# Kernel optimization log

Hardware: AMD Instinct MI355X
Metric: run time of the kernel (lower is better)

## Reference

```python
import jax, jax.numpy as jnp
import numpy as np

D = 256; H = 8; L = 4; K = 4; AS = 2; HD = D // H
KK = K * K
LEVEL_SHAPES = [(128, 128), (64, 64), (32, 32), (16, 16)]


def _kernel_indices():
    # kernel_size=4 (even): linspace(-1.5, 1.5, 4); stack [j, i] then / K
    idx = jnp.linspace(-1.5, 1.5, K)
    ii, jj = jnp.meshgrid(idx, idx, indexing='ij')
    return jnp.stack([jj, ii], axis=-1).reshape(-1, 2) / K  # (KK, 2)


def _bilinear(vf, g, Hl, Wl):
    # vf: (b, H, Hl*Wl, HD) per-level value; g: (b, l1, H, KK, 2) in [0,1]
    # grid_sample semantics, align_corners=False, zero padding
    b, l1, h, kk, _ = g.shape
    x = g[..., 0] * Wl - 0.5
    y = g[..., 1] * Hl - 0.5
    x0 = jnp.floor(x)
    y0 = jnp.floor(y)
    acc = None
    for dx, dy in ((0, 0), (1, 0), (0, 1), (1, 1)):
        xi = x0 + dx
        yi = y0 + dy
        w = (1.0 - jnp.abs(x - xi)) * (1.0 - jnp.abs(y - yi))
        valid = (xi >= 0) & (xi < Wl) & (yi >= 0) & (yi < Hl)
        idx = (jnp.clip(yi, 0, Hl - 1) * Wl + jnp.clip(xi, 0, Wl - 1)).astype(jnp.int32)
        idx = idx.transpose(0, 2, 1, 3).reshape(b, h, l1 * kk)
        gth = jnp.take_along_axis(vf, idx[..., None], axis=2)  # (b,H,l1*kk,HD)
        ww = (w * valid).transpose(0, 2, 1, 3).reshape(b, h, l1 * kk)
        c = gth * ww[..., None]
        acc = c if acc is None else acc + c
    return acc.reshape(b, h, l1, kk, HD).transpose(0, 2, 1, 3, 4)  # (b,l1,H,kk,HD)


def setup_inputs() -> dict:
    key = jax.random.key(0)
    ks = jax.random.split(key, 9)
    b, l1 = 4, 1024
    l2 = sum(h * w for h, w in LEVEL_SHAPES)  # 21760
    query = jax.random.normal(ks[0], (b, l1, D), jnp.float32)
    value = jax.random.normal(ks[1], (b, l2, D), jnp.float32)
    centers = jax.random.uniform(ks[2], (b, l1, 2), jnp.float32)
    sizes = jax.random.uniform(ks[3], (b, l1, 2), jnp.float32) * 0.2 + 0.05
    ref_windows = jnp.concatenate([centers, sizes], axis=-1)  # (b,l1,4) cx,cy,w,h
    s = 1.0 / np.sqrt(D)
    Wv = jax.random.normal(ks[4], (D, D), jnp.float32) * s
    bv = jnp.zeros((D,), jnp.float32)
    Wo = jax.random.normal(ks[5], (D, D), jnp.float32) * s
    bo = jnp.zeros((D,), jnp.float32)
    Wbox = jax.random.normal(ks[6], (L * H * 4, D), jnp.float32) * 0.01
    bbox = jax.random.uniform(ks[7], (H * L * 4,), jnp.float32)
    Wattn = jax.random.normal(ks[8], (H * L * AS * AS, D), jnp.float32) * s
    battn = jnp.zeros((H * L * AS * AS,), jnp.float32)
    v_shape = np.array(LEVEL_SHAPES, np.int64)
    starts = np.cumsum([0] + [h * w for h, w in LEVEL_SHAPES[:-1]])
    v_start_index = np.array(starts, np.int64)
    v_mask = jnp.zeros((b, l2), bool)
    return dict(query=query, value=value, ref_windows=ref_windows, Wv=Wv, bv=bv,
                Wo=Wo, bo=bo, Wbox=Wbox, bbox=bbox, Wattn=Wattn, battn=battn,
                v_shape=v_shape, v_start_index=v_start_index, v_mask=v_mask)


def reference(query, value, ref_windows, Wv, bv, Wo, bo, Wbox, bbox, Wattn, battn,
              v_shape, v_start_index, v_mask):
    b, l1, _ = query.shape
    l2 = value.shape[1]
    # value projection + padding mask
    v = value @ Wv.T + bv
    v = jnp.where(v_mask[..., None], 0.0, v).reshape(b, l2, H, HD)
    # where to attend: offset boxes -> sampling grid (normalizer=None branch)
    off = (query @ Wbox.T + bbox).reshape(b, l1, H, L, 4)
    refw = ref_windows[:, :, None, None, :]            # (b,l1,1,1,4)
    refsz = jnp.concatenate([refw[..., 2:4], refw[..., 2:4]], axis=-1)
    boxes = refw + off / 8.0 * refsz                   # (b,l1,H,L,4)
    center = boxes[..., None, :2]
    size = boxes[..., None, 2:]
    grid = center + _kernel_indices() * jax.nn.relu(size)  # (b,l1,H,L,KK,2)
    # attention weights (attn_size grid upsampled to kernel_size by repeat_interleave)
    aw = (query @ Wattn.T + battn).reshape(b, l1, H, L, AS, AS)
    nr = K // AS
    aw = jnp.repeat(jnp.repeat(aw, nr, axis=-1), nr, axis=-2)  # (b,l1,H,L,K,K)
    sw = jax.nn.softmax(aw.reshape(b, l1, H, -1), axis=-1).reshape(b, l1, H, L, KK)
    lw = jax.nn.softmax(aw, axis=3).reshape(b, l1, H, L, KK)
    out = jnp.zeros((b, l1, H, HD), query.dtype)
    mout = jnp.zeros((b, l1, H, HD), query.dtype)
    for li in range(L):
        Hl, Wl = int(v_shape[li, 0]), int(v_shape[li, 1])
        st = int(v_start_index[li])
        vf = v[:, st:st + Hl * Wl].transpose(0, 2, 1, 3)  # (b,H,Hl*Wl,HD)
        samp = _bilinear(vf, grid[:, :, :, li], Hl, Wl)   # (b,l1,H,KK,HD)
        out = out + jnp.einsum('bqhkd,bqhk->bqhd', samp, sw[:, :, :, li])
        mout = mout + jnp.einsum('bqhkd,bqhk->bqhd', samp, lw[:, :, :, li])
    out = out.reshape(b, l1, D) @ Wo.T + bo
    mout = mout.reshape(b, l1, D) @ Wo.T + bo
    return out, mout, aw
```

## Files before the change

kernel.cpp:

```cpp
#include <hip/hip_runtime.h>
#include <hip/hip_bf16.h>


typedef __attribute__((ext_vector_type(8))) short short8;
typedef __attribute__((ext_vector_type(4))) float f32x4;
typedef __attribute__((ext_vector_type(4))) unsigned int uint4v;

__device__ __forceinline__ unsigned short f2bf(float f) {
    unsigned int u = __float_as_uint(f);
    unsigned int r = u + 0x7FFFu + ((u >> 16) & 1u);
    return (unsigned short)(r >> 16);
}
__device__ __forceinline__ unsigned int pkbf(float a, float b) {
    __hip_bfloat162 h = __float22bfloat162_rn(float2{a, b});
    return *reinterpret_cast<unsigned int*>(&h);
}
__device__ __forceinline__ short8 pack2(float4 x, float4 y) {
    uint4v u;
    u[0] = pkbf(x.x, x.y); u[1] = pkbf(x.z, x.w);
    u[2] = pkbf(y.x, y.y); u[3] = pkbf(y.z, y.w);
    return __builtin_bit_cast(short8, u);
}
__device__ __forceinline__ void gld_lds16(const float* g, float* l) {
    __builtin_amdgcn_global_load_lds(
        (const __attribute__((address_space(1))) unsigned int*)g,
        (__attribute__((address_space(3))) unsigned int*)l, 16, 0, 0);
}

__device__ __forceinline__ void storeC(float* C, size_t i, float v) { C[i] = v; }
__device__ __forceinline__ void storeC(unsigned short* C, size_t i, float v) { C[i] = f2bf(v); }

template <typename OutT>
__device__ __forceinline__ void gemm_body2(
    const float* __restrict__ A, const float* __restrict__ W,
    const float* __restrict__ bias, OutT* __restrict__ C,
    int N, int bm, int bn, float* AsF, float* WsF)
{
    const int tid  = threadIdx.x;
    const int lane = tid & 63;
    const int wave = tid >> 6;
    const int wm = (wave & 1) * 64;
    const int wn = (wave >> 1) * 64;
    const int kg = lane >> 4;
    const int lm = lane & 15;

    f32x4 acc[4][4];
#pragma unroll
    for (int i = 0; i < 4; ++i)
#pragma unroll
        for (int j = 0; j < 4; ++j) {
            acc[i][j][0] = 0.f; acc[i][j][1] = 0.f;
            acc[i][j][2] = 0.f; acc[i][j][3] = 0.f;
        }

    const int g = (lane & 7) ^ (lane >> 3);
    const float* Ag = A + (size_t)(bm + 32 * wave + (lane >> 3)) * 256 + 4 * g;
    const float* Wg = W + (size_t)(bn + 32 * wave + (lane >> 3)) * 256 + 4 * g;
    float* Al = AsF + (32 * wave) * 32;
    float* Wl = WsF + (32 * wave) * 32;

    const int p0 = (2 * kg) ^ (lm & 7);
    const int p1 = p0 ^ 1;
    const float4* Af4 = (const float4*)AsF;
    const float4* Wf4 = (const float4*)WsF;
    const int abase = (wm + lm) * 8;
    const int bbase = (wn + lm) * 8;

    for (int k0 = 0; k0 < 256; k0 += 32) {
        __syncthreads();
#pragma unroll
        for (int j = 0; j < 4; ++j) {
            gld_lds16(Ag + (size_t)j * 8 * 256 + k0, Al + j * 8 * 32);
            gld_lds16(Wg + (size_t)j * 8 * 256 + k0, Wl + j * 8 * 32);
        }
        __syncthreads();
        short8 af[4], bfr[4];
#pragma unroll
        for (int i = 0; i < 4; ++i) {
            float4 c0 = Af4[abase + i * 128 + p0];
            float4 c1 = Af4[abase + i * 128 + p1];
            af[i] = pack2(c0, c1);
        }
#pragma unroll
        for (int j = 0; j < 4; ++j) {
            float4 c0 = Wf4[bbase + j * 128 + p0];
            float4 c1 = Wf4[bbase + j * 128 + p1];
            bfr[j] = pack2(c0, c1);
        }
#pragma unroll
        for (int i = 0; i < 4; ++i)
#pragma unroll
            for (int j = 0; j < 4; ++j)
                acc[i][j] = __builtin_amdgcn_mfma_f32_16x16x32_bf16(
                    af[i], bfr[j], acc[i][j], 0, 0, 0);
    }

#pragma unroll
    for (int j = 0; j < 4; ++j) {
        int col = bn + wn + j * 16 + lm;
        float bcol = bias[col];
#pragma unroll
        for (int i = 0; i < 4; ++i) {
#pragma unroll
            for (int r = 0; r < 4; ++r) {
                int row = bm + wm + i * 16 + kg * 4 + r;
                storeC(C, (size_t)row * N + col, acc[i][j][r] + bcol);
            }
        }
    }
}

#define LDA 56

__device__ __forceinline__ void gemm_body_f32(
    const float* __restrict__ A, const float* __restrict__ W,
    const float* __restrict__ bias, float* __restrict__ C,
    int N, int bm, int bn, unsigned short* As, unsigned short* Ws)
{
    const int tid  = threadIdx.x;
    const int lane = tid & 63;
    const int wave = tid >> 6;
    const int wm = (wave & 1) * 64;
    const int wn = (wave >> 1) * 64;
    const int lr = tid >> 1;
    const int lh = (tid & 1) * 16;
    const int kg = lane >> 4;
    const int lm = lane & 15;

    f32x4 acc[4][4];
#pragma unroll
    for (int i = 0; i < 4; ++i)
#pragma unroll
        for (int j = 0; j < 4; ++j) {
            acc[i][j][0] = 0.f; acc[i][j][1] = 0.f;
            acc[i][j][2] = 0.f; acc[i][j][3] = 0.f;
        }

    const float* Ap = A + (size_t)(bm + lr) * 256 + lh;
    const float* Wp = W + (size_t)(bn + lr) * 256 + lh;
    unsigned short* Asp = &As[lr * LDA + lh];
    unsigned short* Wsp = &Ws[lr * LDA + lh];

    for (int k0 = 0; k0 < 256; k0 += 32) {
        float4 a0 = *(const float4*)(Ap + k0);
        float4 a1 = *(const float4*)(Ap + k0 + 4);
        float4 a2 = *(const float4*)(Ap + k0 + 8);
        float4 a3 = *(const float4*)(Ap + k0 + 12);
        float4 w0 = *(const float4*)(Wp + k0);
        float4 w1 = *(const float4*)(Wp + k0 + 4);
        float4 w2 = *(const float4*)(Wp + k0 + 8);
        float4 w3 = *(const float4*)(Wp + k0 + 12);
        __syncthreads();
        *(short8*)(Asp)     = pack2(a0, a1);
        *(short8*)(Asp + 8) = pack2(a2, a3);
        *(short8*)(Wsp)     = pack2(w0, w1);
        *(short8*)(Wsp + 8) = pack2(w2, w3);
        __syncthreads();
        short8 af[4], bfr[4];
#pragma unroll
        for (int i = 0; i < 4; ++i)
            af[i] = *(const short8*)&As[(wm + i * 16 + lm) * LDA + kg * 8];
#pragma unroll
        for (int j = 0; j < 4; ++j)
            bfr[j] = *(const short8*)&Ws[(wn + j * 16 + lm) * LDA + kg * 8];
#pragma unroll
        for (int i = 0; i < 4; ++i)
#pragma unroll
            for (int j = 0; j < 4; ++j)
                acc[i][j] = __builtin_amdgcn_mfma_f32_16x16x32_bf16(
                    af[i], bfr[j], acc[i][j], 0, 0, 0);
    }

#pragma unroll
    for (int j = 0; j < 4; ++j) {
        int col = bn + wn + j * 16 + lm;
        float bcol = bias[col];
#pragma unroll
        for (int i = 0; i < 4; ++i)
#pragma unroll
            for (int r = 0; r < 4; ++r) {
                int row = bm + wm + i * 16 + kg * 4 + r;
                C[(size_t)row * N + col] = acc[i][j][r] + bcol;
            }
    }
}

__device__ __forceinline__ void gemm_body_bf16A(
    const unsigned short* __restrict__ A, const float* __restrict__ W,
    const float* __restrict__ bias, float* __restrict__ C,
    int N, int bm, int bn, unsigned short* As, unsigned short* Ws)
{
    const int tid  = threadIdx.x;
    const int lane = tid & 63;
    const int wave = tid >> 6;
    const int wm = (wave & 1) * 64;
    const int wn = (wave >> 1) * 64;
    const int lr = tid >> 1;
    const int lh = (tid & 1) * 16;
    const int kg = lane >> 4;
    const int lm = lane & 15;

    f32x4 acc[4][4];
#pragma unroll
    for (int i = 0; i < 4; ++i)
#pragma unroll
        for (int j = 0; j < 4; ++j) {
            acc[i][j][0] = 0.f; acc[i][j][1] = 0.f;
            acc[i][j][2] = 0.f; acc[i][j][3] = 0.f;
        }

    const unsigned short* Ap = A + (size_t)(bm + lr) * 256 + lh;
    const float* Wp = W + (size_t)(bn + lr) * 256 + lh;
    unsigned short* Asp = &As[lr * LDA + lh];
    unsigned short* Wsp = &Ws[lr * LDA + lh];

    for (int k0 = 0; k0 < 256; k0 += 32) {
        uint4v a01 = *(const uint4v*)(Ap + k0);
        uint4v a23 = *(const uint4v*)(Ap + k0 + 8);
        float4 w0 = *(const float4*)(Wp + k0);
        float4 w1 = *(const float4*)(Wp + k0 + 4);
        float4 w2 = *(const float4*)(Wp + k0 + 8);
        float4 w3 = *(const float4*)(Wp + k0 + 12);
        __syncthreads();
        *(short8*)(Asp)     = __builtin_bit_cast(short8, a01);
        *(short8*)(Asp + 8) = __builtin_bit_cast(short8, a23);
        *(short8*)(Wsp)     = pack2(w0, w1);
        *(short8*)(Wsp + 8) = pack2(w2, w3);
        __syncthreads();
        short8 af[4], bfr[4];
#pragma unroll
        for (int i = 0; i < 4; ++i)
            af[i] = *(const short8*)&As[(wm + i * 16 + lm) * LDA + kg * 8];
#pragma unroll
        for (int j = 0; j < 4; ++j)
            bfr[j] = *(const short8*)&Ws[(wn + j * 16 + lm) * LDA + kg * 8];
#pragma unroll
        for (int i = 0; i < 4; ++i)
#pragma unroll
            for (int j = 0; j < 4; ++j)
                acc[i][j] = __builtin_amdgcn_mfma_f32_16x16x32_bf16(
                    af[i], bfr[j], acc[i][j], 0, 0, 0);
    }

#pragma unroll
    for (int j = 0; j < 4; ++j) {
        int col = bn + wn + j * 16 + lm;
        float bcol = bias[col];
#pragma unroll
        for (int i = 0; i < 4; ++i)
#pragma unroll
            for (int r = 0; r < 4; ++r) {
                int row = bm + wm + i * 16 + kg * 4 + r;
                C[(size_t)row * N + col] = acc[i][j][r] + bcol;
            }
    }
}

__global__ __launch_bounds__(256) void gemm_vq_kernel(
    const float* __restrict__ value, const float* __restrict__ Wv,
    const float* __restrict__ bv, unsigned short* __restrict__ v,
    const float* __restrict__ query,
    const float* __restrict__ Wbox, const float* __restrict__ bbox, float* __restrict__ off,
    const float* __restrict__ Wattn, const float* __restrict__ battn, float* __restrict__ awr)
{
    __shared__ __align__(16) char smem[32768];
    const int x = blockIdx.x;
    if (x < 1360) {
        gemm_body2<unsigned short>(value, Wv, bv, v, 256,
                                   (x >> 1) * 128, (x & 1) * 128,
                                   (float*)smem, (float*)(smem + 16384));
    } else {
        const int idx = x - 1360;
        const int bm = (idx & 31) * 128;
        unsigned short* As = (unsigned short*)smem;
        unsigned short* Ws = As + 128 * LDA;
        if (idx < 32) gemm_body_f32(query, Wbox, bbox, off, 128, bm, 0, As, Ws);
        else          gemm_body_f32(query, Wattn, battn, awr, 128, bm, 0, As, Ws);
    }
}

__global__ __launch_bounds__(256) void gemm_o_kernel(
    const unsigned short* __restrict__ A, const float* __restrict__ W,
    const float* __restrict__ bias, float* __restrict__ C)
{
    __shared__ __align__(16) unsigned short As[128 * LDA];
    __shared__ __align__(16) unsigned short Ws[128 * LDA];
    gemm_body_bf16A(A, W, bias, C, 256, blockIdx.x * 128, blockIdx.y * 128, As, Ws);
}

__global__ __launch_bounds__(512, 8) void sample_kernel(
    const unsigned short* __restrict__ v, const float* __restrict__ off,
    const float* __restrict__ awr, const float* __restrict__ refw,
    float* __restrict__ aw_out, unsigned short* __restrict__ accb)
{
    const int x  = blockIdx.x;
    const int bq = ((x & 3) << 10) | (x >> 2);
    const int b  = bq >> 10;
    const int t  = threadIdx.x;

    __shared__ float ref4[4];
    __shared__ float awl[128];
    __shared__ float bxs[128];
    __shared__ float swl[512];
    __shared__ float lwl[512];
    __shared__ int4  tp[32 * 66];

    if (t < 4)   ref4[t] = refw[bq * 4 + t];
    if (t < 128) awl[t] = awr[(size_t)bq * 128 + t];
    __syncthreads();

    if (t < 128) {
        float o = off[(size_t)bq * 128 + t];
        int comp = t & 3;
        float r0 = ref4[0], r1 = ref4[1], r2 = ref4[2], r3 = ref4[3];
        float bx;
        if (comp == 0)      bx = r0 + o * 0.125f * r2;
        else if (comp == 1) bx = r1 + o * 0.125f * r3;
        else if (comp == 2) bx = r2 + o * 0.125f * r2;
        else                bx = r3 + o * 0.125f * r3;
        bxs[t] = bx;

        const int h = t >> 4, r = t & 15;
        float a = awl[t];
        float m = a;
#pragma unroll
        for (int s = 1; s < 16; s <<= 1) m = fmaxf(m, __shfl_xor(m, s, 16));
        float se = expf(a - m);
#pragma unroll
        for (int s = 1; s < 16; s <<= 1) se += __shfl_xor(se, s, 16);
        const float inv_s = 1.0f / (4.0f * se);

        float* awq = aw_out + (size_t)bq * 512 + h * 64;
#pragma unroll
        for (int j = 0; j < 4; ++j) {
            int eidx = r * 4 + j;
            int l  = eidx >> 4;
            int ky = (eidx >> 2) & 3;
            int kx = eidx & 3;
            int pos = (ky >> 1) * 2 + (kx >> 1);
            float raw = awl[h * 16 + l * 4 + pos];
            swl[h * 64 + eidx] = expf(raw - m) * inv_s;
            int base = h * 16 + pos;
            float m2 = awl[base];
#pragma unroll
            for (int li = 1; li < 4; ++li) m2 = fmaxf(m2, awl[base + li * 4]);
            float s2 = 0.f;
#pragma unroll
            for (int li = 0; li < 4; ++li) s2 += expf(awl[base + li * 4] - m2);
            lwl[h * 64 + eidx] = expf(raw - m2) / s2;
            awq[eidx] = raw;
        }
    }
    __syncthreads();

    {
        const int STs_[4] = {0, 16384, 20480, 21504};
        int e = t;
        int eh = e >> 6, rem = e & 63, l = rem >> 4, kk = rem & 15;
        const float* bx = &bxs[eh * 16 + l * 4];
        float cx = bx[0], cy = bx[1];
        float bw = fmaxf(bx[2], 0.f), bh = fmaxf(bx[3], 0.f);
        float kx = -0.375f + 0.25f * (float)(kk & 3);
        float ky = -0.375f + 0.25f * (float)(kk >> 2);
        int Wl = 128 >> l;
        float xg = (cx + kx * bw) * (float)Wl - 0.5f;
        float yg = (cy + ky * bh) * (float)Wl - 0.5f;
        float x0f = floorf(xg), y0f = floorf(yg);
        int x0 = (int)x0f, y0 = (int)y0f;
        float fx = xg - x0f, fy = yg - y0f;
        float sww = swl[e], lww = lwl[e];
        int rowbase = b * 21760 + STs_[l];
        int4* dst = &tp[(eh * 4 + l) * 66 + kk * 4];
#pragma unroll
        for (int tap = 0; tap < 4; ++tap) {
            int dx = tap & 1, dy = tap >> 1;
            int xi = x0 + dx, yi = y0 + dy;
            float w = (dx ? fx : 1.f - fx) * (dy ? fy : 1.f - fy);
            if (xi < 0 || xi >= Wl || yi < 0 || yi >= Wl) w = 0.f;
            int xc = min(max(xi, 0), Wl - 1);
            int yc = min(max(yi, 0), Wl - 1);
            dst[tap] = int4{(rowbase + yc * Wl + xc) << 6,
                            __float_as_int(w * sww),
                            __float_as_int(w * lww), 0};
        }
    }
    __syncthreads();

    const int h    = t >> 6;
    const int lane = t & 63;
    const int l    = (lane >> 4) & 3;
    const int sub  = (lane >> 3) & 1;
    const int cl   = lane & 7;
    const uint2* vp = (const uint2*)v;
    const int choff = h * 8 + cl;
    const int4* sp = &tp[(h * 4 + l) * 66 + sub];

    float a0 = 0.f, a1 = 0.f, a2 = 0.f, a3 = 0.f;
    float m0 = 0.f, m1 = 0.f, m2 = 0.f, m3 = 0.f;
#pragma unroll 4
    for (int i = 0; i < 32; ++i) {
        int4 d = sp[2 * i];
        uint2 pv = vp[(size_t)(d.x + choff)];
        float v0 = __uint_as_float(pv.x << 16);
        float v1 = __uint_as_float(pv.x & 0xffff0000u);
        float v2 = __uint_as_float(pv.y << 16);
        float v3 = __uint_as_float(pv.y & 0xffff0000u);
        float wo = __int_as_float(d.y), wm = __int_as_float(d.z);
        a0 = fmaf(v0, wo, a0); a1 = fmaf(v1, wo, a1);
        a2 = fmaf(v2, wo, a2); a3 = fmaf(v3, wo, a3);
        m0 = fmaf(v0, wm, m0); m1 = fmaf(v1, wm, m1);
        m2 = fmaf(v2, wm, m2); m3 = fmaf(v3, wm, m3);
    }
#pragma unroll
    for (int s = 8; s <= 32; s <<= 1) {
        a0 += __shfl_xor(a0, s); a1 += __shfl_xor(a1, s);
        a2 += __shfl_xor(a2, s); a3 += __shfl_xor(a3, s);
        m0 += __shfl_xor(m0, s); m1 += __shfl_xor(m1, s);
        m2 += __shfl_xor(m2, s); m3 += __shfl_xor(m3, s);
    }
    if (lane < 8) {
        size_t base = (size_t)bq * 256 + h * 32 + cl * 4;
        *(uint2*)&accb[base] = uint2{pkbf(a0, a1), pkbf(a2, a3)};
        *(uint2*)&accb[base + (size_t)4096 * 256] = uint2{pkbf(m0, m1), pkbf(m2, m3)};
    }
}

extern "C" void kernel_launch(void* const* d_in, const int* in_sizes, int n_in,
                              void* d_out, int out_size, void* d_ws, size_t ws_size,
                              hipStream_t stream) {
    const float* query = (const float*)d_in[0];
    const float* value = (const float*)d_in[1];
    const float* refw  = (const float*)d_in[2];
    const float* Wv    = (const float*)d_in[3];
    const float* bv    = (const float*)d_in[4];
    const float* Wo    = (const float*)d_in[5];
    const float* bo    = (const float*)d_in[6];
    const float* Wbox  = (const float*)d_in[7];
    const float* bbox  = (const float*)d_in[8];
    const float* Wattn = (const float*)d_in[9];
    const float* battn = (const float*)d_in[10];

    float* out = (float*)d_out;
    float* aw_out = out + 2 * 1048576;

    unsigned short* v = (unsigned short*)d_ws;
    float* off = (float*)((char*)d_ws + 44564480);
    float* awr = off + 524288;
    unsigned short* accb = (unsigned short*)(awr + 524288);

    gemm_vq_kernel<<<1424, 256, 0, stream>>>(value, Wv, bv, v,
                                             query, Wbox, bbox, off,
                                             Wattn, battn, awr);
    sample_kernel<<<4096, 512, 0, stream>>>(v, off, awr, refw, aw_out, accb);
    gemm_o_kernel<<<dim3(64, 2), 256, 0, stream>>>(accb, Wo, bo, out);
}
```

Baseline: 250.2 us.

## Double-buffer LDS tiles in value projection GEMM to overlap loads with MFMA

```diff
diff --git a/kernel.cpp b/kernel.cpp
--- a/kernel.cpp
+++ b/kernel.cpp
@@ -29,6 +29,8 @@
 
 __device__ __forceinline__ void storeC(float* C, size_t i, float v) { C[i] = v; }
 __device__ __forceinline__ void storeC(unsigned short* C, size_t i, float v) { C[i] = f2bf(v); }
+
+#define TILE_F 4096
 
 template <typename OutT>
 __device__ __forceinline__ void gemm_body2(
@@ -56,24 +58,37 @@
     const int g = (lane & 7) ^ (lane >> 3);
     const float* Ag = A + (size_t)(bm + 32 * wave + (lane >> 3)) * 256 + 4 * g;
     const float* Wg = W + (size_t)(bn + 32 * wave + (lane >> 3)) * 256 + 4 * g;
-    float* Al = AsF + (32 * wave) * 32;
-    float* Wl = WsF + (32 * wave) * 32;
+    const int ldsw = (32 * wave) * 32;
 
     const int p0 = (2 * kg) ^ (lm & 7);
     const int p1 = p0 ^ 1;
-    const float4* Af4 = (const float4*)AsF;
-    const float4* Wf4 = (const float4*)WsF;
     const int abase = (wm + lm) * 8;
     const int bbase = (wn + lm) * 8;
 
-    for (int k0 = 0; k0 < 256; k0 += 32) {
-        __syncthreads();
-#pragma unroll
-        for (int j = 0; j < 4; ++j) {
-            gld_lds16(Ag + (size_t)j * 8 * 256 + k0, Al + j * 8 * 32);
-            gld_lds16(Wg + (size_t)j * 8 * 256 + k0, Wl + j * 8 * 32);
-        }
-        __syncthreads();
+#pragma unroll
+    for (int j = 0; j < 4; ++j) {
+        gld_lds16(Ag + (size_t)j * 8 * 256, AsF + ldsw + j * 8 * 32);
+        gld_lds16(Wg + (size_t)j * 8 * 256, WsF + ldsw + j * 8 * 32);
+    }
+    asm volatile("s_waitcnt vmcnt(0)" ::: "memory");
+    __builtin_amdgcn_s_barrier();
+
+#pragma unroll 2
+    for (int it = 0; it < 8; ++it) {
+        const int cur = it & 1;
+        const int nxt = cur ^ 1;
+        if (it < 7) {
+            const int k0 = 32 * (it + 1);
+#pragma unroll
+            for (int j = 0; j < 4; ++j) {
+                gld_lds16(Ag + (size_t)j * 8 * 256 + k0,
+                          AsF + nxt * TILE_F + ldsw + j * 8 * 32);
+                gld_lds16(Wg + (size_t)j * 8 * 256 + k0,
+                          WsF + nxt * TILE_F + ldsw + j * 8 * 32);
+            }
+        }
+        const float4* Af4 = (const float4*)(AsF + cur * TILE_F);
+        const float4* Wf4 = (const float4*)(WsF + cur * TILE_F);
         short8 af[4], bfr[4];
 #pragma unroll
         for (int i = 0; i < 4; ++i) {
@@ -93,6 +108,11 @@
             for (int j = 0; j < 4; ++j)
                 acc[i][j] = __builtin_amdgcn_mfma_f32_16x16x32_bf16(
                     af[i], bfr[j], acc[i][j], 0, 0, 0);
+        if (it < 7) {
+            asm volatile("s_waitcnt vmcnt(0) lgkmcnt(0)" ::: "memory");
+            __builtin_amdgcn_s_barrier();
+            asm volatile("" ::: "memory");
+        }
     }
 
 #pragma unroll
@@ -263,12 +283,12 @@
     const float* __restrict__ Wbox, const float* __restrict__ bbox, float* __restrict__ off,
     const float* __restrict__ Wattn, const float* __restrict__ battn, float* __restrict__ awr)
 {
-    __shared__ __align__(16) char smem[32768];
+    __shared__ __align__(16) char smem[65536];
     const int x = blockIdx.x;
     if (x < 1360) {
         gemm_body2<unsigned short>(value, Wv, bv, v, 256,
                                    (x >> 1) * 128, (x & 1) * 128,
-                                   (float*)smem, (float*)(smem + 16384));
+                                   (float*)smem, (float*)(smem + 32768));
     } else {
         const int idx = x - 1360;
         const int bm = (idx & 31) * 128;
```

Result: no change. 245.3 us (-1.9%).

## Register-prefetch value GEMM tiles, store bf16 in double-buffered LDS

Applied to the files above, without the earlier changes.

```diff
diff --git a/kernel.cpp b/kernel.cpp
--- a/kernel.cpp
+++ b/kernel.cpp
@@ -21,20 +21,15 @@
     u[2] = pkbf(y.x, y.y); u[3] = pkbf(y.z, y.w);
     return __builtin_bit_cast(short8, u);
 }
-__device__ __forceinline__ void gld_lds16(const float* g, float* l) {
-    __builtin_amdgcn_global_load_lds(
-        (const __attribute__((address_space(1))) unsigned int*)g,
-        (__attribute__((address_space(3))) unsigned int*)l, 16, 0, 0);
-}
 
 __device__ __forceinline__ void storeC(float* C, size_t i, float v) { C[i] = v; }
 __device__ __forceinline__ void storeC(unsigned short* C, size_t i, float v) { C[i] = f2bf(v); }
 
 template <typename OutT>
-__device__ __forceinline__ void gemm_body2(
+__device__ __forceinline__ void gemm_body3(
     const float* __restrict__ A, const float* __restrict__ W,
     const float* __restrict__ bias, OutT* __restrict__ C,
-    int N, int bm, int bn, float* AsF, float* WsF)
+    int N, int bm, int bn, char* smem)
 {
     const int tid  = threadIdx.x;
     const int lane = tid & 63;
@@ -44,6 +39,9 @@
     const int kg = lane >> 4;
     const int lm = lane & 15;
 
+    char* ldsA = smem;
+    char* ldsW = smem + 16384;
+
     f32x4 acc[4][4];
 #pragma unroll
     for (int i = 0; i < 4; ++i)
@@ -53,47 +51,59 @@
             acc[i][j][2] = 0.f; acc[i][j][3] = 0.f;
         }
 
-    const int g = (lane & 7) ^ (lane >> 3);
-    const float* Ag = A + (size_t)(bm + 32 * wave + (lane >> 3)) * 256 + 4 * g;
-    const float* Wg = W + (size_t)(bn + 32 * wave + (lane >> 3)) * 256 + 4 * g;
-    float* Al = AsF + (32 * wave) * 32;
-    float* Wl = WsF + (32 * wave) * 32;
-
-    const int p0 = (2 * kg) ^ (lm & 7);
-    const int p1 = p0 ^ 1;
-    const float4* Af4 = (const float4*)AsF;
-    const float4* Wf4 = (const float4*)WsF;
-    const int abase = (wm + lm) * 8;
-    const int bbase = (wn + lm) * 8;
-
-    for (int k0 = 0; k0 < 256; k0 += 32) {
+    const int prow = tid >> 1;
+    const int ph   = tid & 1;
+    const float* Ag = A + (size_t)(bm + prow) * 256 + ph * 16;
+    const float* Wg = W + (size_t)(bn + prow) * 256 + ph * 16;
+    const int f   = (prow >> 1) & 3;
+    const int pp  = ph ^ (f >> 1);
+    const int wlo = (f & 1) * 16;
+    const int whi = wlo ^ 16;
+    char* wA = ldsA + prow * 64 + pp * 32;
+    char* wW = ldsW + prow * 64 + pp * 32;
+
+    const int aslot = (kg ^ ((lm >> 1) & 3)) * 16;
+    const int aoff  = (wm + lm) * 64 + aslot;
+    const int woff  = (wn + lm) * 64 + aslot;
+
+    float4 fa[4], fw[4];
+#define ISSUE_VQ(K0)                                          \
+    {                                                         \
+        _Pragma("unroll")                                     \
+        for (int q = 0; q < 4; ++q) {                         \
+            fa[q] = *(const float4*)(Ag + (K0) + 4 * q);      \
+            fw[q] = *(const float4*)(Wg + (K0) + 4 * q);      \
+        }                                                     \
+    }
+
+    ISSUE_VQ(0)
+
+    for (int it = 0; it < 8; ++it) {
+        const int b = it & 1;
+        char* wAb = wA + b * 8192;
+        char* wWb = wW + b * 8192;
+        *(short8*)(wAb + wlo) = pack2(fa[0], fa[1]);
+        *(short8*)(wAb + whi) = pack2(fa[2], fa[3]);
+        *(short8*)(wWb + wlo) = pack2(fw[0], fw[1]);
+        *(short8*)(wWb + whi) = pack2(fw[2], fw[3]);
         __syncthreads();
+        if (it < 7) ISSUE_VQ(32 * (it + 1))
+        const char* bA = ldsA + b * 8192;
+        const char* bW = ldsW + b * 8192;
+        short8 af[4];
+#pragma unroll
+        for (int i = 0; i < 4; ++i)
+            af[i] = *(const short8*)(bA + aoff + i * 1024);
 #pragma unroll
         for (int j = 0; j < 4; ++j) {
-            gld_lds16(Ag + (size_t)j * 8 * 256 + k0, Al + j * 8 * 32);
-            gld_lds16(Wg + (size_t)j * 8 * 256 + k0, Wl + j * 8 * 32);
-        }
-        __syncthreads();
-        short8 af[4], bfr[4];
-#pragma unroll
-        for (int i = 0; i < 4; ++i) {
-            float4 c0 = Af4[abase + i * 128 + p0];
-            float4 c1 = Af4[abase + i * 128 + p1];
-            af[i] = pack2(c0, c1);
-        }
-#pragma unroll
-        for (int j = 0; j < 4; ++j) {
-            float4 c0 = Wf4[bbase + j * 128 + p0];
-            float4 c1 = Wf4[bbase + j * 128 + p1];
-            bfr[j] = pack2(c0, c1);
-        }
-#pragma unroll
-        for (int i = 0; i < 4; ++i)
-#pragma unroll
-            for (int j = 0; j < 4; ++j)
+            short8 bf = *(const short8*)(bW + woff + j * 1024);
+#pragma unroll
+            for (int i = 0; i < 4; ++i)
                 acc[i][j] = __builtin_amdgcn_mfma_f32_16x16x32_bf16(
-                    af[i], bfr[j], acc[i][j], 0, 0, 0);
-    }
+                    af[i], bf, acc[i][j], 0, 0, 0);
+        }
+    }
+#undef ISSUE_VQ
 
 #pragma unroll
     for (int j = 0; j < 4; ++j) {
@@ -256,7 +266,7 @@
     }
 }
 
-__global__ __launch_bounds__(256) void gemm_vq_kernel(
+__global__ __launch_bounds__(256, 4) void gemm_vq_kernel(
     const float* __restrict__ value, const float* __restrict__ Wv,
     const float* __restrict__ bv, unsigned short* __restrict__ v,
     const float* __restrict__ query,
@@ -266,9 +276,8 @@
     __shared__ __align__(16) char smem[32768];
     const int x = blockIdx.x;
     if (x < 1360) {
-        gemm_body2<unsigned short>(value, Wv, bv, v, 256,
-                                   (x >> 1) * 128, (x & 1) * 128,
-                                   (float*)smem, (float*)(smem + 16384));
+        gemm_body3<unsigned short>(value, Wv, bv, v, 256,
+                                   (x >> 1) * 128, (x & 1) * 128, smem);
     } else {
         const int idx = x - 1360;
         const int bm = (idx & 31) * 128;
```

After: 250.2 us. No clear change (+0.0%).

## Store projected value in head-major layout and load GEMM operands directly to registers

Applied to the files above, without the earlier changes.

```diff
diff --git a/kernel.cpp b/kernel.cpp
--- a/kernel.cpp
+++ b/kernel.cpp
@@ -21,20 +21,11 @@
     u[2] = pkbf(y.x, y.y); u[3] = pkbf(y.z, y.w);
     return __builtin_bit_cast(short8, u);
 }
-__device__ __forceinline__ void gld_lds16(const float* g, float* l) {
-    __builtin_amdgcn_global_load_lds(
-        (const __attribute__((address_space(1))) unsigned int*)g,
-        (__attribute__((address_space(3))) unsigned int*)l, 16, 0, 0);
-}
-
-__device__ __forceinline__ void storeC(float* C, size_t i, float v) { C[i] = v; }
-__device__ __forceinline__ void storeC(unsigned short* C, size_t i, float v) { C[i] = f2bf(v); }
-
-template <typename OutT>
-__device__ __forceinline__ void gemm_body2(
+
+__device__ __forceinline__ void gemm_body_v(
     const float* __restrict__ A, const float* __restrict__ W,
-    const float* __restrict__ bias, OutT* __restrict__ C,
-    int N, int bm, int bn, float* AsF, float* WsF)
+    const float* __restrict__ bias, unsigned short* __restrict__ C,
+    int bm, int bn, int vb, int pbase, char* smem)
 {
     const int tid  = threadIdx.x;
     const int lane = tid & 63;
@@ -53,39 +44,35 @@
             acc[i][j][2] = 0.f; acc[i][j][3] = 0.f;
         }
 
-    const int g = (lane & 7) ^ (lane >> 3);
-    const float* Ag = A + (size_t)(bm + 32 * wave + (lane >> 3)) * 256 + 4 * g;
-    const float* Wg = W + (size_t)(bn + 32 * wave + (lane >> 3)) * 256 + 4 * g;
-    float* Al = AsF + (32 * wave) * 32;
-    float* Wl = WsF + (32 * wave) * 32;
-
-    const int p0 = (2 * kg) ^ (lm & 7);
-    const int p1 = p0 ^ 1;
-    const float4* Af4 = (const float4*)AsF;
-    const float4* Wf4 = (const float4*)WsF;
-    const int abase = (wm + lm) * 8;
-    const int bbase = (wn + lm) * 8;
-
-    for (int k0 = 0; k0 < 256; k0 += 32) {
-        __syncthreads();
-#pragma unroll
-        for (int j = 0; j < 4; ++j) {
-            gld_lds16(Ag + (size_t)j * 8 * 256 + k0, Al + j * 8 * 32);
-            gld_lds16(Wg + (size_t)j * 8 * 256 + k0, Wl + j * 8 * 32);
-        }
-        __syncthreads();
+    const float* Arow = A + (size_t)(bm + wm + lm) * 256 + kg * 8;
+    const float* Wrow = W + (size_t)(bn + wn + lm) * 256 + kg * 8;
+
+    float4 ca[8], cw[8];
+#pragma unroll
+    for (int q = 0; q < 4; ++q) {
+        ca[2 * q]     = *(const float4*)(Arow + q * 4096);
+        ca[2 * q + 1] = *(const float4*)(Arow + q * 4096 + 4);
+        cw[2 * q]     = *(const float4*)(Wrow + q * 4096);
+        cw[2 * q + 1] = *(const float4*)(Wrow + q * 4096 + 4);
+    }
+
+#pragma unroll
+    for (int it = 0; it < 8; ++it) {
         short8 af[4], bfr[4];
 #pragma unroll
-        for (int i = 0; i < 4; ++i) {
-            float4 c0 = Af4[abase + i * 128 + p0];
-            float4 c1 = Af4[abase + i * 128 + p1];
-            af[i] = pack2(c0, c1);
-        }
-#pragma unroll
-        for (int j = 0; j < 4; ++j) {
-            float4 c0 = Wf4[bbase + j * 128 + p0];
-            float4 c1 = Wf4[bbase + j * 128 + p1];
-            bfr[j] = pack2(c0, c1);
+        for (int q = 0; q < 4; ++q) {
+            af[q]  = pack2(ca[2 * q], ca[2 * q + 1]);
+            bfr[q] = pack2(cw[2 * q], cw[2 * q + 1]);
+        }
+        if (it < 7) {
+            const int k0 = 32 * (it + 1);
+#pragma unroll
+            for (int q = 0; q < 4; ++q) {
+                ca[2 * q]     = *(const float4*)(Arow + q * 4096 + k0);
+                ca[2 * q + 1] = *(const float4*)(Arow + q * 4096 + k0 + 4);
+                cw[2 * q]     = *(const float4*)(Wrow + q * 4096 + k0);
+                cw[2 * q + 1] = *(const float4*)(Wrow + q * 4096 + k0 + 4);
+            }
         }
 #pragma unroll
         for (int i = 0; i < 4; ++i)
@@ -95,17 +82,33 @@
                     af[i], bfr[j], acc[i][j], 0, 0, 0);
     }
 
-#pragma unroll
-    for (int j = 0; j < 4; ++j) {
-        int col = bn + wn + j * 16 + lm;
-        float bcol = bias[col];
-#pragma unroll
-        for (int i = 0; i < 4; ++i) {
-#pragma unroll
-            for (int r = 0; r < 4; ++r) {
-                int row = bm + wm + i * 16 + kg * 4 + r;
-                storeC(C, (size_t)row * N + col, acc[i][j][r] + bcol);
+    {
+        unsigned short* sv = (unsigned short*)smem;
+#pragma unroll
+        for (int j = 0; j < 4; ++j) {
+            const int cb = wn + j * 16;
+            const int pl = cb >> 5;
+            const int ch = (cb & 16) + lm;
+            const float bcol = bias[bn + cb + lm];
+#pragma unroll
+            for (int i = 0; i < 4; ++i) {
+#pragma unroll
+                for (int r = 0; r < 4; ++r) {
+                    const int px = wm + i * 16 + kg * 4 + r;
+                    sv[(pl * 128 + px) * 32 + ch] = f2bf(acc[i][j][r] + bcol);
+                }
             }
+        }
+    }
+    __syncthreads();
+    {
+        const unsigned short* sv = (const unsigned short*)smem;
+        const int plbase = vb * 8 + (bn >> 5);
+#pragma unroll
+        for (int q = 0; q < 8; ++q) {
+            size_t gbase = ((size_t)(plbase + (q >> 1)) * 21760 + pbase) * 32
+                         + (q & 1) * 2048 + tid * 8;
+            *(uint4v*)&C[gbase] = *(const uint4v*)&sv[q * 2048 + tid * 8];
         }
     }
 }
@@ -266,9 +269,11 @@
     __shared__ __align__(16) char smem[32768];
     const int x = blockIdx.x;
     if (x < 1360) {
-        gemm_body2<unsigned short>(value, Wv, bv, v, 256,
-                                   (x >> 1) * 128, (x & 1) * 128,
-                                   (float*)smem, (float*)(smem + 16384));
+        const int rb = x >> 1;
+        const int vb = rb / 170;
+        const int pbase = (rb - vb * 170) * 128;
+        gemm_body_v(value, Wv, bv, v, rb * 128, (x & 1) * 128,
+                    vb, pbase, smem);
     } else {
         const int idx = x - 1360;
         const int bm = (idx & 31) * 128;
@@ -369,7 +374,7 @@
         int x0 = (int)x0f, y0 = (int)y0f;
         float fx = xg - x0f, fy = yg - y0f;
         float sww = swl[e], lww = lwl[e];
-        int rowbase = b * 21760 + STs_[l];
+        int rowbase = (b * 8 + eh) * 21760 + STs_[l];
         int4* dst = &tp[(eh * 4 + l) * 66 + kk * 4];
 #pragma unroll
         for (int tap = 0; tap < 4; ++tap) {
@@ -379,7 +384,7 @@
             if (xi < 0 || xi >= Wl || yi < 0 || yi >= Wl) w = 0.f;
             int xc = min(max(xi, 0), Wl - 1);
             int yc = min(max(yi, 0), Wl - 1);
-            dst[tap] = int4{(rowbase + yc * Wl + xc) << 6,
+            dst[tap] = int4{(rowbase + yc * Wl + xc) << 3,
                             __float_as_int(w * sww),
                             __float_as_int(w * lww), 0};
         }
@@ -392,7 +397,6 @@
     const int sub  = (lane >> 3) & 1;
     const int cl   = lane & 7;
     const uint2* vp = (const uint2*)v;
-    const int choff = h * 8 + cl;
     const int4* sp = &tp[(h * 4 + l) * 66 + sub];
 
     float a0 = 0.f, a1 = 0.f, a2 = 0.f, a3 = 0.f;
@@ -400,7 +404,7 @@
 #pragma unroll 4
     for (int i = 0; i < 32; ++i) {
         int4 d = sp[2 * i];
-        uint2 pv = vp[(size_t)(d.x + choff)];
+        uint2 pv = vp[(size_t)(d.x + cl)];
         float v0 = __uint_as_float(pv.x << 16);
         float v1 = __uint_as_float(pv.x & 0xffff0000u);
         float v2 = __uint_as_float(pv.y << 16);
```

After: 292.6 us. +17.0%, slower.
